# Performance work log

Hardware: AMD Instinct MI355X
Metric: run time of the kernel (lower is better)

## Reference

```python
import jax, jax.numpy as jnp
import numpy as np

N = 50000
E = 500000
HID = 128
H = 4
D = HID // H
NUM_EDGE_TYPES = 8
EPS_LN = 1e-5


def setup_inputs() -> dict:
    key = jax.random.key(0)
    ks = jax.random.split(key, 16)
    s = 1.0 / np.sqrt(HID)
    return {
        "node_embeddings": jax.random.normal(ks[0], (N, HID), jnp.float32),
        "edge_index": jax.random.randint(ks[1], (2, E), 0, N, jnp.int32),
        "edge_type": jax.random.randint(ks[2], (E,), 0, NUM_EDGE_TYPES, jnp.int32),
        "task_embedding": jax.random.normal(ks[3], (HID,), jnp.float32),
        "W_src": jax.random.normal(ks[4], (HID, HID), jnp.float32) * s,
        "b_src": jnp.zeros((HID,), jnp.float32),
        "W_dst": jax.random.normal(ks[5], (HID, HID), jnp.float32) * s,
        "b_dst": jnp.zeros((HID,), jnp.float32),
        "edge_emb": jax.random.normal(ks[6], (NUM_EDGE_TYPES, HID), jnp.float32),
        "att": jax.random.normal(ks[7], (H, D), jnp.float32) * s,
        "W_out": jax.random.normal(ks[8], (HID, HID), jnp.float32) * s,
        "b_out": jnp.zeros((HID,), jnp.float32),
        "norm_w": jnp.ones((HID,), jnp.float32),
        "norm_b": jnp.zeros((HID,), jnp.float32),
        "W_film": jax.random.normal(ks[9], (HID, 2 * HID), jnp.float32) * s,
        "b_film": jnp.zeros((2 * HID,), jnp.float32),
    }


def reference(node_embeddings, edge_index, edge_type, task_embedding,
              W_src, b_src, W_dst, b_dst, edge_emb, att,
              W_out, b_out, norm_w, norm_b, W_film, b_film):
    num_nodes = node_embeddings.shape[0]
    src, dst = edge_index[0], edge_index[1]

    # Node projections -> [N, H, D]
    x_src = (node_embeddings @ W_src + b_src).reshape(num_nodes, H, D)
    x_dst = (node_embeddings @ W_dst + b_dst).reshape(num_nodes, H, D)
    e = edge_emb[edge_type].reshape(-1, H, D)  # [E, H, D]

    # GATv2 attention logits per edge per head
    combined = jax.nn.leaky_relu(x_src[src] + x_dst[dst] + e, negative_slope=0.2)
    logits = jnp.einsum('ehd,hd->eh', combined, att)  # [E, H]

    # Scatter-softmax over destination nodes
    mx = jax.ops.segment_max(logits, dst, num_segments=num_nodes)  # [N, H]
    mx = jnp.where(jnp.isinf(mx), jnp.zeros_like(mx), mx)
    ex = jnp.exp(logits - mx[dst])
    sums = jax.ops.segment_sum(ex, dst, num_segments=num_nodes)  # [N, H]
    attn = ex / jnp.maximum(sums[dst], 1e-12)  # [E, H]

    # Weighted message aggregation
    msg = x_src[src] * attn[..., None]  # [E, H, D]
    agg = jax.ops.segment_sum(msg, dst, num_segments=num_nodes)  # [N, H, D]
    agg = agg.reshape(num_nodes, HID) @ W_out + b_out

    # Task FiLM modulation
    film = task_embedding @ W_film + b_film  # [2*HID]
    gamma, beta = film[:HID], film[HID:]
    agg = agg * (1.0 + 0.5 * jnp.tanh(gamma))[None, :] + beta[None, :]

    # Residual + LayerNorm
    y = node_embeddings + agg
    mu = jnp.mean(y, axis=-1, keepdims=True)
    var = jnp.mean((y - mu) ** 2, axis=-1, keepdims=True)
    return (y - mu) / jnp.sqrt(var + EPS_LN) * norm_w + norm_b
```

## Files before the change

### kernel.cpp

```cpp
#include <hip/hip_runtime.h>
#include <hip/hip_bf16.h>

#define N_NODES 50000
#define E_EDGES 500000
#define HID 128
#define NHEAD 4
#define HDIM 32
#define SCAN_BLOCKS ((N_NODES + 255) / 256)

typedef __attribute__((ext_vector_type(8))) short bf16x8;
typedef __attribute__((ext_vector_type(8))) unsigned short u16x8;
typedef __attribute__((ext_vector_type(4))) float f32x4;

static __device__ __forceinline__ float b2f(unsigned short u) {
    return __uint_as_float((unsigned int)u << 16);
}
static __device__ __forceinline__ unsigned short f2b(float f) {
    unsigned int u = __float_as_uint(f);
    u += 0x7FFFu + ((u >> 16) & 1u);
    return (unsigned short)(u >> 16);
}

__global__ __launch_bounds__(256) void film_kernel(
    const float* __restrict__ task, const float* __restrict__ Wf,
    const float* __restrict__ bf, float* __restrict__ film)
{
    __shared__ float tsk[HID];
    const int t = threadIdx.x;
    if (t < HID) tsk[t] = task[t];
    __syncthreads();
    float acc = bf[t];
    #pragma unroll 8
    for (int k = 0; k < HID; ++k)
        acc = fmaf(tsk[k], Wf[k * 256 + t], acc);
    if (t < HID) film[t] = 1.f + 0.5f * tanhf(acc);
    else         film[t] = acc;
}

__global__ __launch_bounds__(256) void prep_weights(
    const float* __restrict__ Ws, const float* __restrict__ Wd,
    unsigned short* __restrict__ B1)
{
    const int id = blockIdx.x * 256 + threadIdx.x;
    const int n = id >> 7;
    const int k = id & 127;
    const float v = (n < HID) ? Ws[(size_t)k * HID + n]
                              : Wd[(size_t)k * HID + (n - HID)];
    size_t byte = ((size_t)n * HID + k) * 2;
    byte ^= (size_t)((n & 7) << 4);
    *(unsigned short*)((char*)B1 + byte) = f2b(v);
}

__global__ __launch_bounds__(256) void gemm_mfma(
    const float* __restrict__ A, const unsigned short* __restrict__ B1,
    const float* __restrict__ bs, const float* __restrict__ bd,
    unsigned short* __restrict__ xs, unsigned short* __restrict__ xd)
{
    __shared__ unsigned short a_lds[64 * HID];
    __shared__ unsigned short b_lds[256 * HID];
    const int t  = threadIdx.x;
    const int nb = blockIdx.x * 64;

    #pragma unroll
    for (int i = 0; i < 8; ++i) {
        const int f   = t + 256 * i;
        const int row = f >> 5;
        const int k4  = f & 31;
        const int node = nb + row;
        float4 v;
        if (node < N_NODES) v = *(const float4*)(A + (size_t)node * HID + k4 * 4);
        else { v.x = v.y = v.z = v.w = 0.f; }
        ushort4 h;
        h.x = f2b(v.x); h.y = f2b(v.y); h.z = f2b(v.z); h.w = f2b(v.w);
        int byte = row * 256 + k4 * 8;
        byte ^= (row & 7) << 4;
        *(ushort4*)((char*)a_lds + byte) = h;
    }
    #pragma unroll
    for (int i = 0; i < 16; ++i) {
        const int off = (t + 256 * i) * 8;
        const u16x8 v = *(const u16x8*)(B1 + off);
        *(u16x8*)(b_lds + off) = v;
    }
    __syncthreads();

    const int w   = t >> 6;
    const int l   = t & 63;
    const int l15 = l & 15;
    const int kg  = l >> 4;

    f32x4 acc[4][4];
    #pragma unroll
    for (int mf = 0; mf < 4; ++mf)
        #pragma unroll
        for (int nf = 0; nf < 4; ++nf) acc[mf][nf] = (f32x4){0.f, 0.f, 0.f, 0.f};

    #pragma unroll
    for (int ks = 0; ks < 4; ++ks) {
        bf16x8 af[4], bfg[4];
        #pragma unroll
        for (int mf = 0; mf < 4; ++mf) {
            const int r = mf * 16 + l15;
            int byte = r * 256 + ks * 64 + kg * 16;
            byte ^= (r & 7) << 4;
            af[mf] = *(const bf16x8*)((const char*)a_lds + byte);
        }
        #pragma unroll
        for (int nf = 0; nf < 4; ++nf) {
            const int rb = w * 64 + nf * 16 + l15;
            int byte = rb * 256 + ks * 64 + kg * 16;
            byte ^= (rb & 7) << 4;
            bfg[nf] = *(const bf16x8*)((const char*)b_lds + byte);
        }
        #pragma unroll
        for (int mf = 0; mf < 4; ++mf)
            #pragma unroll
            for (int nf = 0; nf < 4; ++nf)
                acc[mf][nf] = __builtin_amdgcn_mfma_f32_16x16x32_bf16(
                    af[mf], bfg[nf], acc[mf][nf], 0, 0, 0);
    }

    float bias[4];
    #pragma unroll
    for (int nf = 0; nf < 4; ++nf) {
        const int col = w * 64 + nf * 16 + l15;
        bias[nf] = (col < HID) ? bs[col] : bd[col - HID];
    }

    __syncthreads();
    unsigned short* c_lds = b_lds;

    #pragma unroll
    for (int mf = 0; mf < 4; ++mf)
        #pragma unroll
        for (int nf = 0; nf < 4; ++nf) {
            const int col = w * 64 + nf * 16 + l15;
            #pragma unroll
            for (int j = 0; j < 4; ++j) {
                const int row = mf * 16 + kg * 4 + j;
                c_lds[row * 264 + col] = f2b(acc[mf][nf][j] + bias[nf]);
            }
        }
    __syncthreads();

    #pragma unroll
    for (int p = 0; p < 8; ++p) {
        const int row   = p * 8 + (t >> 5);
        const int chunk = t & 31;
        const int node  = nb + row;
        if (node < N_NODES) {
            const u16x8 v = *(const u16x8*)(c_lds + row * 264 + chunk * 8);
            if (chunk < 16)
                *(u16x8*)(xs + (size_t)node * HID + chunk * 8) = v;
            else
                *(u16x8*)(xd + (size_t)node * HID + (chunk - 16) * 8) = v;
        }
    }
}

__global__ __launch_bounds__(256) void hist_kernel(
    const int* __restrict__ ei, int* __restrict__ deg)
{
    const int e = blockIdx.x * 256 + threadIdx.x;
    if (e < E_EDGES) atomicAdd(&deg[ei[E_EDGES + e]], 1);
}

__global__ __launch_bounds__(256) void reduce_blocks(
    const int* __restrict__ deg, int* __restrict__ blocksum)
{
    __shared__ int ws_[4];
    const int t = threadIdx.x;
    const int i = blockIdx.x * 256 + t;
    int v = (i < N_NODES) ? deg[i] : 0;
    #pragma unroll
    for (int off = 32; off; off >>= 1) v += __shfl_down(v, off);
    if ((t & 63) == 0) ws_[t >> 6] = v;
    __syncthreads();
    if (t == 0) blocksum[blockIdx.x] = ws_[0] + ws_[1] + ws_[2] + ws_[3];
}

__global__ __launch_bounds__(256) void scan_blocksums(
    const int* __restrict__ blocksum, int* __restrict__ blockoff,
    int* __restrict__ rowptr)
{
    __shared__ int wtot[4];
    const int t    = threadIdx.x;
    const int lane = t & 63;
    const int w    = t >> 6;
    int v = (t < SCAN_BLOCKS) ? blocksum[t] : 0;
    const int own = v;
    #pragma unroll
    for (int off = 1; off < 64; off <<= 1) {
        const int u = __shfl_up(v, off);
        if (lane >= off) v += u;
    }
    if (lane == 63) wtot[w] = v;
    __syncthreads();
    int woff = 0;
    #pragma unroll
    for (int k = 0; k < 4; ++k) if (k < w) woff += wtot[k];
    if (t < SCAN_BLOCKS) blockoff[t] = woff + v - own;
    if (t == 0) rowptr[N_NODES] = E_EDGES;
}

__global__ __launch_bounds__(256) void scan_within(
    const int* __restrict__ deg, const int* __restrict__ blockoff,
    int* __restrict__ rowptr, int* __restrict__ cursor)
{
    __shared__ int wtot[4];
    const int t    = threadIdx.x;
    const int lane = t & 63;
    const int w    = t >> 6;
    const int i    = blockIdx.x * 256 + t;
    int v = (i < N_NODES) ? deg[i] : 0;
    const int own = v;
    #pragma unroll
    for (int off = 1; off < 64; off <<= 1) {
        const int u = __shfl_up(v, off);
        if (lane >= off) v += u;
    }
    if (lane == 63) wtot[w] = v;
    __syncthreads();
    int woff = blockoff[blockIdx.x];
    #pragma unroll
    for (int k = 0; k < 4; ++k) if (k < w) woff += wtot[k];
    if (i < N_NODES) {
        const int ex = woff + v - own;
        rowptr[i] = ex;
        cursor[i] = ex;
    }
}

__global__ __launch_bounds__(256) void scatter_kernel(
    const int* __restrict__ ei, const int* __restrict__ et,
    int* __restrict__ cursor, int* __restrict__ pack)
{
    const int e = blockIdx.x * 256 + threadIdx.x;
    if (e < E_EDGES) {
        const int d = ei[E_EDGES + e];
        const int pos = atomicAdd(&cursor[d], 1);
        pack[pos] = ei[e] | (et[e] << 16);
    }
}

__global__ __launch_bounds__(256) void gather_agg(
    const int* __restrict__ rowptr, const int* __restrict__ pack,
    const unsigned short* __restrict__ xsrc,
    const unsigned short* __restrict__ xdst,
    const float* __restrict__ eemb, const float* __restrict__ att,
    float* __restrict__ agg)
{
    const int lane = threadIdx.x & 31;
    const int grp  = threadIdx.x >> 5;
    const int node = blockIdx.x * 8 + grp;
    if (node >= N_NODES) return;

    const float4 av = *(const float4*)(att + lane * 4);
    const ushort4 xdu = *(const ushort4*)(xdst + (size_t)node * HID + lane * 4);
    const float xdx = b2f(xdu.x), xdy = b2f(xdu.y),
                xdz = b2f(xdu.z), xdw = b2f(xdu.w);

    float a0 = 0.f, a1 = 0.f, a2 = 0.f, a3 = 0.f, sum = 0.f;
    const int b = rowptr[node];
    const int e = rowptr[node + 1];

    int i = b;
    for (; i + 1 < e; i += 2) {
        const int pk0 = pack[i];
        const int pk1 = pack[i + 1];
        const int s0 = pk0 & 0xFFFF, ty0 = pk0 >> 16;
        const int s1 = pk1 & 0xFFFF, ty1 = pk1 >> 16;
        const ushort4 u0 = *(const ushort4*)(xsrc + (size_t)s0 * HID + lane * 4);
        const float4  ev0 = *(const float4*)(eemb + (size_t)ty0 * HID + lane * 4);
        const ushort4 u1 = *(const ushort4*)(xsrc + (size_t)s1 * HID + lane * 4);
        const float4  ev1 = *(const float4*)(eemb + (size_t)ty1 * HID + lane * 4);
        const float x0x = b2f(u0.x), x0y = b2f(u0.y), x0z = b2f(u0.z), x0w = b2f(u0.w);
        const float x1x = b2f(u1.x), x1y = b2f(u1.y), x1z = b2f(u1.z), x1w = b2f(u1.w);
        float c, p0 = 0.f, p1 = 0.f;
        c = x0x + xdx + ev0.x; c = (c > 0.f) ? c : 0.2f * c; p0 = fmaf(c, av.x, p0);
        c = x0y + xdy + ev0.y; c = (c > 0.f) ? c : 0.2f * c; p0 = fmaf(c, av.y, p0);
        c = x0z + xdz + ev0.z; c = (c > 0.f) ? c : 0.2f * c; p0 = fmaf(c, av.z, p0);
        c = x0w + xdw + ev0.w; c = (c > 0.f) ? c : 0.2f * c; p0 = fmaf(c, av.w, p0);
        c = x1x + xdx + ev1.x; c = (c > 0.f) ? c : 0.2f * c; p1 = fmaf(c, av.x, p1);
        c = x1y + xdy + ev1.y; c = (c > 0.f) ? c : 0.2f * c; p1 = fmaf(c, av.y, p1);
        c = x1z + xdz + ev1.z; c = (c > 0.f) ? c : 0.2f * c; p1 = fmaf(c, av.z, p1);
        c = x1w + xdw + ev1.w; c = (c > 0.f) ? c : 0.2f * c; p1 = fmaf(c, av.w, p1);
        p0 += __shfl_xor(p0, 1); p1 += __shfl_xor(p1, 1);
        p0 += __shfl_xor(p0, 2); p1 += __shfl_xor(p1, 2);
        p0 += __shfl_xor(p0, 4); p1 += __shfl_xor(p1, 4);
        const float ex0 = expf(p0);
        const float ex1 = expf(p1);
        a0 = fmaf(ex0, x0x, a0); a1 = fmaf(ex0, x0y, a1);
        a2 = fmaf(ex0, x0z, a2); a3 = fmaf(ex0, x0w, a3);
        a0 = fmaf(ex1, x1x, a0); a1 = fmaf(ex1, x1y, a1);
        a2 = fmaf(ex1, x1z, a2); a3 = fmaf(ex1, x1w, a3);
        sum += ex0 + ex1;
    }
    if (i < e) {
        const int pk0 = pack[i];
        const int s0 = pk0 & 0xFFFF, ty0 = pk0 >> 16;
        const ushort4 u0 = *(const ushort4*)(xsrc + (size_t)s0 * HID + lane * 4);
        const float4  ev0 = *(const float4*)(eemb + (size_t)ty0 * HID + lane * 4);
        const float x0x = b2f(u0.x), x0y = b2f(u0.y), x0z = b2f(u0.z), x0w = b2f(u0.w);
        float c, p0 = 0.f;
        c = x0x + xdx + ev0.x; c = (c > 0.f) ? c : 0.2f * c; p0 = fmaf(c, av.x, p0);
        c = x0y + xdy + ev0.y; c = (c > 0.f) ? c : 0.2f * c; p0 = fmaf(c, av.y, p0);
        c = x0z + xdz + ev0.z; c = (c > 0.f) ? c : 0.2f * c; p0 = fmaf(c, av.z, p0);
        c = x0w + xdw + ev0.w; c = (c > 0.f) ? c : 0.2f * c; p0 = fmaf(c, av.w, p0);
        p0 += __shfl_xor(p0, 1);
        p0 += __shfl_xor(p0, 2);
        p0 += __shfl_xor(p0, 4);
        const float ex0 = expf(p0);
        a0 = fmaf(ex0, x0x, a0); a1 = fmaf(ex0, x0y, a1);
        a2 = fmaf(ex0, x0z, a2); a3 = fmaf(ex0, x0w, a3);
        sum += ex0;
    }

    const float inv = 1.f / fmaxf(sum, 1e-12f);
    float4 o;
    o.x = a0 * inv; o.y = a1 * inv; o.z = a2 * inv; o.w = a3 * inv;
    *(float4*)(agg + (size_t)node * HID + lane * 4) = o;
}

__global__ __launch_bounds__(256) void finalize(
    const float* __restrict__ agg,
    const float* __restrict__ A,   const float* __restrict__ Wo,
    const float* __restrict__ bo,  const float* __restrict__ film,
    const float* __restrict__ nw_, const float* __restrict__ nb_,
    float* __restrict__ out)
{
    __shared__ float a_tile[64][HID];
    const int t  = threadIdx.x;
    const int nb = blockIdx.x * 64;

    #pragma unroll
    for (int i = 0; i < 8; ++i) {
        int f  = t + 256 * i;
        int m  = f >> 5;
        int k4 = f & 31;
        int node = nb + m;
        float4 v;
        if (node < N_NODES) v = *(const float4*)(agg + (size_t)node * HID + k4 * 4);
        else { v.x = v.y = v.z = v.w = 0.f; }
        *(float4*)&a_tile[m][k4 * 4] = v;
    }
    __syncthreads();

    const int cg = t & 31;
    const int rg = t >> 5;
    const int cc = cg * 4;
    const int m0 = rg * 8;

    float acc[8][4];
    #pragma unroll
    for (int m = 0; m < 8; ++m)
        #pragma unroll
        for (int j = 0; j < 4; ++j) acc[m][j] = 0.f;

    for (int kc = 0; kc < 32; ++kc) {
        const int k0 = kc * 4;
        const float4 w0 = *(const float4*)(Wo + (size_t)(k0 + 0) * HID + cc);
        const float4 w1 = *(const float4*)(Wo + (size_t)(k0 + 1) * HID + cc);
        const float4 w2 = *(const float4*)(Wo + (size_t)(k0 + 2) * HID + cc);
        const float4 w3 = *(const float4*)(Wo + (size_t)(k0 + 3) * HID + cc);
        #pragma unroll
        for (int m = 0; m < 8; ++m) {
            const float4 av = *(const float4*)&a_tile[m0 + m][k0];
            acc[m][0] = fmaf(av.x, w0.x, acc[m][0]);
            acc[m][1] = fmaf(av.x, w0.y, acc[m][1]);
            acc[m][2] = fmaf(av.x, w0.z, acc[m][2]);
            acc[m][3] = fmaf(av.x, w0.w, acc[m][3]);
            acc[m][0] = fmaf(av.y, w1.x, acc[m][0]);
            acc[m][1] = fmaf(av.y, w1.y, acc[m][1]);
            acc[m][2] = fmaf(av.y, w1.z, acc[m][2]);
            acc[m][3] = fmaf(av.y, w1.w, acc[m][3]);
            acc[m][0] = fmaf(av.z, w2.x, acc[m][0]);
            acc[m][1] = fmaf(av.z, w2.y, acc[m][1]);
            acc[m][2] = fmaf(av.z, w2.z, acc[m][2]);
            acc[m][3] = fmaf(av.z, w2.w, acc[m][3]);
            acc[m][0] = fmaf(av.w, w3.x, acc[m][0]);
            acc[m][1] = fmaf(av.w, w3.y, acc[m][1]);
            acc[m][2] = fmaf(av.w, w3.z, acc[m][2]);
            acc[m][3] = fmaf(av.w, w3.w, acc[m][3]);
        }
    }

    const float4 bv  = *(const float4*)(bo   + cc);
    const float4 gfv = *(const float4*)(film + cc);
    const float4 btv = *(const float4*)(film + HID + cc);
    const float4 nwv = *(const float4*)(nw_  + cc);
    const float4 nbv = *(const float4*)(nb_  + cc);

    #pragma unroll
    for (int m = 0; m < 8; ++m) {
        const int node = nb + m0 + m;
        float4 y;
        float4 r;
        if (node < N_NODES) r = *(const float4*)(A + (size_t)node * HID + cc);
        else { r.x = r.y = r.z = r.w = 0.f; }
        y.x = fmaf(acc[m][0] + bv.x, gfv.x, btv.x) + r.x;
        y.y = fmaf(acc[m][1] + bv.y, gfv.y, btv.y) + r.y;
        y.z = fmaf(acc[m][2] + bv.z, gfv.z, btv.z) + r.z;
        y.w = fmaf(acc[m][3] + bv.w, gfv.w, btv.w) + r.w;

        float s1 = y.x + y.y + y.z + y.w;
        float s2 = y.x * y.x + y.y * y.y + y.z * y.z + y.w * y.w;
        #pragma unroll
        for (int off = 1; off < 32; off <<= 1) {
            s1 += __shfl_xor(s1, off);
            s2 += __shfl_xor(s2, off);
        }
        const float mu   = s1 * (1.f / 128.f);
        const float var  = s2 * (1.f / 128.f) - mu * mu;
        const float rsig = rsqrtf(var + 1e-5f);
        if (node < N_NODES) {
            float4 o;
            o.x = (y.x - mu) * rsig * nwv.x + nbv.x;
            o.y = (y.y - mu) * rsig * nwv.y + nbv.y;
            o.z = (y.z - mu) * rsig * nwv.z + nbv.z;
            o.w = (y.w - mu) * rsig * nwv.w + nbv.w;
            *(float4*)(out + (size_t)node * HID + cc) = o;
        }
    }
}

extern "C" void kernel_launch(void* const* d_in, const int* in_sizes, int n_in,
                              void* d_out, int out_size, void* d_ws, size_t ws_size,
                              hipStream_t stream)
{
    const float* node_emb = (const float*)d_in[0];
    const int*   edge_idx = (const int*)  d_in[1];
    const int*   edge_ty  = (const int*)  d_in[2];
    const float* task     = (const float*)d_in[3];
    const float* W_src    = (const float*)d_in[4];
    const float* b_src    = (const float*)d_in[5];
    const float* W_dst    = (const float*)d_in[6];
    const float* b_dst    = (const float*)d_in[7];
    const float* edge_emb = (const float*)d_in[8];
    const float* att      = (const float*)d_in[9];
    const float* W_out    = (const float*)d_in[10];
    const float* b_out    = (const float*)d_in[11];
    const float* norm_w   = (const float*)d_in[12];
    const float* norm_b   = (const float*)d_in[13];
    const float* W_film   = (const float*)d_in[14];
    const float* b_film   = (const float*)d_in[15];
    float* out = (float*)d_out;

    char* ws = (char*)d_ws;
    float* agg      = (float*)ws;                            ws += (size_t)N_NODES * HID * 4;
    float* film     = (float*)ws;                            ws += 256 * 4;
    int*   deg      = (int*)ws;                              ws += (size_t)N_NODES * 4;
    int*   rowptr   = (int*)ws;                              ws += (size_t)(N_NODES + 4) * 4;
    int*   cursor   = (int*)ws;                              ws += (size_t)N_NODES * 4;
    int*   blocksum = (int*)ws;                              ws += 256 * 4;
    int*   blockoff = (int*)ws;                              ws += 256 * 4;
    int*   pack     = (int*)ws;                              ws += (size_t)E_EDGES * 4;
    unsigned short* x_src = (unsigned short*)ws;             ws += (size_t)N_NODES * HID * 2;
    unsigned short* x_dst = (unsigned short*)ws;             ws += (size_t)N_NODES * HID * 2;
    unsigned short* wb1   = (unsigned short*)ws;             ws += (size_t)256 * HID * 2;

    hipMemsetAsync(deg, 0, (size_t)N_NODES * sizeof(int), stream);

    film_kernel<<<1, 256, 0, stream>>>(task, W_film, b_film, film);
    hist_kernel<<<(E_EDGES + 255) / 256, 256, 0, stream>>>(edge_idx, deg);
    prep_weights<<<(256 * HID) / 256, 256, 0, stream>>>(W_src, W_dst, wb1);
    gemm_mfma<<<(N_NODES + 63) / 64, 256, 0, stream>>>(
        node_emb, wb1, b_src, b_dst, x_src, x_dst);
    reduce_blocks<<<SCAN_BLOCKS, 256, 0, stream>>>(deg, blocksum);
    scan_blocksums<<<1, 256, 0, stream>>>(blocksum, blockoff, rowptr);
    scan_within<<<SCAN_BLOCKS, 256, 0, stream>>>(deg, blockoff, rowptr, cursor);
    scatter_kernel<<<(E_EDGES + 255) / 256, 256, 0, stream>>>(
        edge_idx, edge_ty, cursor, pack);
    gather_agg<<<(N_NODES + 7) / 8, 256, 0, stream>>>(
        rowptr, pack, x_src, x_dst, edge_emb, att, agg);
    finalize<<<(N_NODES + 63) / 64, 256, 0, stream>>>(
        agg, node_emb, W_out, b_out, film, norm_w, norm_b, out);
}
```

Before: 255.8 us.

## Use split-bf16 MFMA for output projection and merge prep kernels

Moves the finalize kernel's fp32 scalar GEMM onto MFMA using a hi/lo bf16 split (three MFMAs per tile) with pre-transposed, swizzled W_out halves prepared once. Merges the film and weight-prep kernels into a single launch, and makes the histogram and scatter kernels process two edges per thread with int2 loads. Also replaces the leaky-relu select with fmaxf. The split-bf16 product drops the lo*lo term, so results differ slightly from fp32, and finalize now uses more LDS.

```diff
diff --git a/kernel.cpp b/kernel.cpp
--- a/kernel.cpp
+++ b/kernel.cpp
@@ -5,7 +5,6 @@
 #define E_EDGES 500000
 #define HID 128
 #define NHEAD 4
-#define HDIM 32
 #define SCAN_BLOCKS ((N_NODES + 255) / 256)
 
 typedef __attribute__((ext_vector_type(8))) short bf16x8;
@@ -21,34 +20,57 @@
     return (unsigned short)(u >> 16);
 }
 
-__global__ __launch_bounds__(256) void film_kernel(
+__global__ __launch_bounds__(256) void prep_kernel(
+    const float* __restrict__ Ws, const float* __restrict__ Wd,
+    const float* __restrict__ Wo,
     const float* __restrict__ task, const float* __restrict__ Wf,
-    const float* __restrict__ bf, float* __restrict__ film)
-{
-    __shared__ float tsk[HID];
+    const float* __restrict__ bfi,
+    unsigned short* __restrict__ B1,
+    unsigned short* __restrict__ B2h, unsigned short* __restrict__ B2l,
+    float* __restrict__ film)
+{
+    const int blk = blockIdx.x;
     const int t = threadIdx.x;
-    if (t < HID) tsk[t] = task[t];
-    __syncthreads();
-    float acc = bf[t];
-    #pragma unroll 8
-    for (int k = 0; k < HID; ++k)
-        acc = fmaf(tsk[k], Wf[k * 256 + t], acc);
-    if (t < HID) film[t] = 1.f + 0.5f * tanhf(acc);
-    else         film[t] = acc;
-}
-
-__global__ __launch_bounds__(256) void prep_weights(
-    const float* __restrict__ Ws, const float* __restrict__ Wd,
-    unsigned short* __restrict__ B1)
-{
-    const int id = blockIdx.x * 256 + threadIdx.x;
-    const int n = id >> 7;
-    const int k = id & 127;
-    const float v = (n < HID) ? Ws[(size_t)k * HID + n]
-                              : Wd[(size_t)k * HID + (n - HID)];
-    size_t byte = ((size_t)n * HID + k) * 2;
-    byte ^= (size_t)((n & 7) << 4);
-    *(unsigned short*)((char*)B1 + byte) = f2b(v);
+    if (blk < 256) {
+        const int id = blk * 256 + t;
+        if (id < 256 * HID) {
+            const int n = id >> 7;
+            const int k = id & 127;
+            const float v = (n < HID) ? Ws[(size_t)k * HID + n]
+                                      : Wd[(size_t)k * HID + (n - HID)];
+            size_t byte = ((size_t)n * HID + k) * 2;
+            byte ^= (size_t)((n & 7) << 4);
+            *(unsigned short*)((char*)B1 + byte) = f2b(v);
+        } else if (id < 256 * HID + HID * HID) {
+            const int id2 = id - 256 * HID;
+            const int n = id2 >> 7;
+            const int k = id2 & 127;
+            const float v = Wo[(size_t)k * HID + n];
+            size_t byte = ((size_t)n * HID + k) * 2;
+            byte ^= (size_t)((n & 7) << 4);
+            *(unsigned short*)((char*)B2h + byte) = f2b(v);
+        } else {
+            const int id3 = id - 256 * HID - HID * HID;
+            const int n = id3 >> 7;
+            const int k = id3 & 127;
+            const float v = Wo[(size_t)k * HID + n];
+            const unsigned short hi = f2b(v);
+            const unsigned short lo = f2b(v - b2f(hi));
+            size_t byte = ((size_t)n * HID + k) * 2;
+            byte ^= (size_t)((n & 7) << 4);
+            *(unsigned short*)((char*)B2l + byte) = lo;
+        }
+    } else {
+        __shared__ float tsk[HID];
+        if (t < HID) tsk[t] = task[t];
+        __syncthreads();
+        float acc = bfi[t];
+        #pragma unroll 8
+        for (int k = 0; k < HID; ++k)
+            acc = fmaf(tsk[k], Wf[k * 256 + t], acc);
+        if (t < HID) film[t] = 1.f + 0.5f * tanhf(acc);
+        else         film[t] = acc;
+    }
 }
 
 __global__ __launch_bounds__(256) void gemm_mfma(
@@ -161,8 +183,13 @@
 __global__ __launch_bounds__(256) void hist_kernel(
     const int* __restrict__ ei, int* __restrict__ deg)
 {
-    const int e = blockIdx.x * 256 + threadIdx.x;
-    if (e < E_EDGES) atomicAdd(&deg[ei[E_EDGES + e]], 1);
+    const int e2 = blockIdx.x * 256 + threadIdx.x;
+    const int e = e2 * 2;
+    if (e < E_EDGES) {
+        const int2 d = *(const int2*)(ei + E_EDGES + e);
+        atomicAdd(&deg[d.x], 1);
+        if (e + 1 < E_EDGES) atomicAdd(&deg[d.y], 1);
+    }
 }
 
 __global__ __launch_bounds__(256) void reduce_blocks(
@@ -235,11 +262,18 @@
     const int* __restrict__ ei, const int* __restrict__ et,
     int* __restrict__ cursor, int* __restrict__ pack)
 {
-    const int e = blockIdx.x * 256 + threadIdx.x;
+    const int e2 = blockIdx.x * 256 + threadIdx.x;
+    const int e = e2 * 2;
     if (e < E_EDGES) {
-        const int d = ei[E_EDGES + e];
-        const int pos = atomicAdd(&cursor[d], 1);
-        pack[pos] = ei[e] | (et[e] << 16);
+        const int2 s  = *(const int2*)(ei + e);
+        const int2 d  = *(const int2*)(ei + E_EDGES + e);
+        const int2 ty = *(const int2*)(et + e);
+        const int p0 = atomicAdd(&cursor[d.x], 1);
+        pack[p0] = s.x | (ty.x << 16);
+        if (e + 1 < E_EDGES) {
+            const int p1 = atomicAdd(&cursor[d.y], 1);
+            pack[p1] = s.y | (ty.y << 16);
+        }
     }
 }
 
@@ -277,14 +311,14 @@
         const float x0x = b2f(u0.x), x0y = b2f(u0.y), x0z = b2f(u0.z), x0w = b2f(u0.w);
         const float x1x = b2f(u1.x), x1y = b2f(u1.y), x1z = b2f(u1.z), x1w = b2f(u1.w);
         float c, p0 = 0.f, p1 = 0.f;
-        c = x0x + xdx + ev0.x; c = (c > 0.f) ? c : 0.2f * c; p0 = fmaf(c, av.x, p0);
-        c = x0y + xdy + ev0.y; c = (c > 0.f) ? c : 0.2f * c; p0 = fmaf(c, av.y, p0);
-        c = x0z + xdz + ev0.z; c = (c > 0.f) ? c : 0.2f * c; p0 = fmaf(c, av.z, p0);
-        c = x0w + xdw + ev0.w; c = (c > 0.f) ? c : 0.2f * c; p0 = fmaf(c, av.w, p0);
-        c = x1x + xdx + ev1.x; c = (c > 0.f) ? c : 0.2f * c; p1 = fmaf(c, av.x, p1);
-        c = x1y + xdy + ev1.y; c = (c > 0.f) ? c : 0.2f * c; p1 = fmaf(c, av.y, p1);
-        c = x1z + xdz + ev1.z; c = (c > 0.f) ? c : 0.2f * c; p1 = fmaf(c, av.z, p1);
-        c = x1w + xdw + ev1.w; c = (c > 0.f) ? c : 0.2f * c; p1 = fmaf(c, av.w, p1);
+        c = x0x + xdx + ev0.x; c = fmaxf(c, 0.2f * c); p0 = fmaf(c, av.x, p0);
+        c = x0y + xdy + ev0.y; c = fmaxf(c, 0.2f * c); p0 = fmaf(c, av.y, p0);
+        c = x0z + xdz + ev0.z; c = fmaxf(c, 0.2f * c); p0 = fmaf(c, av.z, p0);
+        c = x0w + xdw + ev0.w; c = fmaxf(c, 0.2f * c); p0 = fmaf(c, av.w, p0);
+        c = x1x + xdx + ev1.x; c = fmaxf(c, 0.2f * c); p1 = fmaf(c, av.x, p1);
+        c = x1y + xdy + ev1.y; c = fmaxf(c, 0.2f * c); p1 = fmaf(c, av.y, p1);
+        c = x1z + xdz + ev1.z; c = fmaxf(c, 0.2f * c); p1 = fmaf(c, av.z, p1);
+        c = x1w + xdw + ev1.w; c = fmaxf(c, 0.2f * c); p1 = fmaf(c, av.w, p1);
         p0 += __shfl_xor(p0, 1); p1 += __shfl_xor(p1, 1);
         p0 += __shfl_xor(p0, 2); p1 += __shfl_xor(p1, 2);
         p0 += __shfl_xor(p0, 4); p1 += __shfl_xor(p1, 4);
@@ -303,10 +337,10 @@
         const float4  ev0 = *(const float4*)(eemb + (size_t)ty0 * HID + lane * 4);
         const float x0x = b2f(u0.x), x0y = b2f(u0.y), x0z = b2f(u0.z), x0w = b2f(u0.w);
         float c, p0 = 0.f;
-        c = x0x + xdx + ev0.x; c = (c > 0.f) ? c : 0.2f * c; p0 = fmaf(c, av.x, p0);
-        c = x0y + xdy + ev0.y; c = (c > 0.f) ? c : 0.2f * c; p0 = fmaf(c, av.y, p0);
-        c = x0z + xdz + ev0.z; c = (c > 0.f) ? c : 0.2f * c; p0 = fmaf(c, av.z, p0);
-        c = x0w + xdw + ev0.w; c = (c > 0.f) ? c : 0.2f * c; p0 = fmaf(c, av.w, p0);
+        c = x0x + xdx + ev0.x; c = fmaxf(c, 0.2f * c); p0 = fmaf(c, av.x, p0);
+        c = x0y + xdy + ev0.y; c = fmaxf(c, 0.2f * c); p0 = fmaf(c, av.y, p0);
+        c = x0z + xdz + ev0.z; c = fmaxf(c, 0.2f * c); p0 = fmaf(c, av.z, p0);
+        c = x0w + xdw + ev0.w; c = fmaxf(c, 0.2f * c); p0 = fmaf(c, av.w, p0);
         p0 += __shfl_xor(p0, 1);
         p0 += __shfl_xor(p0, 2);
         p0 += __shfl_xor(p0, 4);
@@ -324,66 +358,112 @@
 
 __global__ __launch_bounds__(256) void finalize(
     const float* __restrict__ agg,
-    const float* __restrict__ A,   const float* __restrict__ Wo,
-    const float* __restrict__ bo,  const float* __restrict__ film,
+    const unsigned short* __restrict__ B2h,
+    const unsigned short* __restrict__ B2l,
+    const float* __restrict__ A,   const float* __restrict__ bo,
+    const float* __restrict__ film,
     const float* __restrict__ nw_, const float* __restrict__ nb_,
     float* __restrict__ out)
 {
-    __shared__ float a_tile[64][HID];
+    __shared__ unsigned short a_hi[64 * HID];
+    __shared__ unsigned short a_lo[64 * HID];
+    __shared__ __align__(16) unsigned short b_pair[2 * HID * HID];
+    float* c_lds = (float*)b_pair;
+    unsigned short* b_hi = b_pair;
+    unsigned short* b_lo = b_pair + HID * HID;
+
     const int t  = threadIdx.x;
     const int nb = blockIdx.x * 64;
 
     #pragma unroll
     for (int i = 0; i < 8; ++i) {
-        int f  = t + 256 * i;
-        int m  = f >> 5;
-        int k4 = f & 31;
-        int node = nb + m;
+        const int f   = t + 256 * i;
+        const int row = f >> 5;
+        const int k4  = f & 31;
+        const int node = nb + row;
         float4 v;
         if (node < N_NODES) v = *(const float4*)(agg + (size_t)node * HID + k4 * 4);
         else { v.x = v.y = v.z = v.w = 0.f; }
-        *(float4*)&a_tile[m][k4 * 4] = v;
-    }
+        ushort4 h, lo;
+        h.x = f2b(v.x); lo.x = f2b(v.x - b2f(h.x));
+        h.y = f2b(v.y); lo.y = f2b(v.y - b2f(h.y));
+        h.z = f2b(v.z); lo.z = f2b(v.z - b2f(h.z));
+        h.w = f2b(v.w); lo.w = f2b(v.w - b2f(h.w));
+        int byte = row * 256 + k4 * 8;
+        byte ^= (row & 7) << 4;
+        *(ushort4*)((char*)a_hi + byte) = h;
+        *(ushort4*)((char*)a_lo + byte) = lo;
+    }
+    #pragma unroll
+    for (int i = 0; i < 8; ++i) {
+        const int off = (t + 256 * i) * 8;
+        *(u16x8*)(b_hi + off) = *(const u16x8*)(B2h + off);
+        *(u16x8*)(b_lo + off) = *(const u16x8*)(B2l + off);
+    }
+    __syncthreads();
+
+    const int w   = t >> 6;
+    const int l   = t & 63;
+    const int l15 = l & 15;
+    const int kg  = l >> 4;
+
+    f32x4 acc[4][2];
+    #pragma unroll
+    for (int mf = 0; mf < 4; ++mf)
+        #pragma unroll
+        for (int nf = 0; nf < 2; ++nf) acc[mf][nf] = (f32x4){0.f, 0.f, 0.f, 0.f};
+
+    #pragma unroll
+    for (int ks = 0; ks < 4; ++ks) {
+        bf16x8 afh[4], afl[4], bfh[2], bfl[2];
+        #pragma unroll
+        for (int mf = 0; mf < 4; ++mf) {
+            const int r = mf * 16 + l15;
+            int byte = r * 256 + ks * 64 + kg * 16;
+            byte ^= (r & 7) << 4;
+            afh[mf] = *(const bf16x8*)((const char*)a_hi + byte);
+            afl[mf] = *(const bf16x8*)((const char*)a_lo + byte);
+        }
+        #pragma unroll
+        for (int nf = 0; nf < 2; ++nf) {
+            const int rb = w * 32 + nf * 16 + l15;
+            int byte = rb * 256 + ks * 64 + kg * 16;
+            byte ^= (rb & 7) << 4;
+            bfh[nf] = *(const bf16x8*)((const char*)b_hi + byte);
+            bfl[nf] = *(const bf16x8*)((const char*)b_lo + byte);
+        }
+        #pragma unroll
+        for (int mf = 0; mf < 4; ++mf)
+            #pragma unroll
+            for (int nf = 0; nf < 2; ++nf) {
+                acc[mf][nf] = __builtin_amdgcn_mfma_f32_16x16x32_bf16(
+                    afh[mf], bfh[nf], acc[mf][nf], 0, 0, 0);
+                acc[mf][nf] = __builtin_amdgcn_mfma_f32_16x16x32_bf16(
+                    afh[mf], bfl[nf], acc[mf][nf], 0, 0, 0);
+                acc[mf][nf] = __builtin_amdgcn_mfma_f32_16x16x32_bf16(
+                    afl[mf], bfh[nf], acc[mf][nf], 0, 0, 0);
+            }
+    }
+
+    __syncthreads();
+
+    #pragma unroll
+    for (int mf = 0; mf < 4; ++mf)
+        #pragma unroll
+        for (int nf = 0; nf < 2; ++nf) {
+            const int col = w * 32 + nf * 16 + l15;
+            #pragma unroll
+            for (int j = 0; j < 4; ++j) {
+                const int row = mf * 16 + kg * 4 + j;
+                c_lds[row * 132 + col] = acc[mf][nf][j];
+            }
+        }
     __syncthreads();
 
     const int cg = t & 31;
     const int rg = t >> 5;
     const int cc = cg * 4;
     const int m0 = rg * 8;
-
-    float acc[8][4];
-    #pragma unroll
-    for (int m = 0; m < 8; ++m)
-        #pragma unroll
-        for (int j = 0; j < 4; ++j) acc[m][j] = 0.f;
-
-    for (int kc = 0; kc < 32; ++kc) {
-        const int k0 = kc * 4;
-        const float4 w0 = *(const float4*)(Wo + (size_t)(k0 + 0) * HID + cc);
-        const float4 w1 = *(const float4*)(Wo + (size_t)(k0 + 1) * HID + cc);
-        const float4 w2 = *(const float4*)(Wo + (size_t)(k0 + 2) * HID + cc);
-        const float4 w3 = *(const float4*)(Wo + (size_t)(k0 + 3) * HID + cc);
-        #pragma unroll
-        for (int m = 0; m < 8; ++m) {
-            const float4 av = *(const float4*)&a_tile[m0 + m][k0];
-            acc[m][0] = fmaf(av.x, w0.x, acc[m][0]);
-            acc[m][1] = fmaf(av.x, w0.y, acc[m][1]);
-            acc[m][2] = fmaf(av.x, w0.z, acc[m][2]);
-            acc[m][3] = fmaf(av.x, w0.w, acc[m][3]);
-            acc[m][0] = fmaf(av.y, w1.x, acc[m][0]);
-            acc[m][1] = fmaf(av.y, w1.y, acc[m][1]);
-            acc[m][2] = fmaf(av.y, w1.z, acc[m][2]);
-            acc[m][3] = fmaf(av.y, w1.w, acc[m][3]);
-            acc[m][0] = fmaf(av.z, w2.x, acc[m][0]);
-            acc[m][1] = fmaf(av.z, w2.y, acc[m][1]);
-            acc[m][2] = fmaf(av.z, w2.z, acc[m][2]);
-            acc[m][3] = fmaf(av.z, w2.w, acc[m][3]);
-            acc[m][0] = fmaf(av.w, w3.x, acc[m][0]);
-            acc[m][1] = fmaf(av.w, w3.y, acc[m][1]);
-            acc[m][2] = fmaf(av.w, w3.z, acc[m][2]);
-            acc[m][3] = fmaf(av.w, w3.w, acc[m][3]);
-        }
-    }
 
     const float4 bv  = *(const float4*)(bo   + cc);
     const float4 gfv = *(const float4*)(film + cc);
@@ -393,15 +473,17 @@
 
     #pragma unroll
     for (int m = 0; m < 8; ++m) {
-        const int node = nb + m0 + m;
-        float4 y;
+        const int row  = m0 + m;
+        const int node = nb + row;
+        const float4 cv = *(const float4*)&c_lds[row * 132 + cc];
         float4 r;
         if (node < N_NODES) r = *(const float4*)(A + (size_t)node * HID + cc);
         else { r.x = r.y = r.z = r.w = 0.f; }
-        y.x = fmaf(acc[m][0] + bv.x, gfv.x, btv.x) + r.x;
-        y.y = fmaf(acc[m][1] + bv.y, gfv.y, btv.y) + r.y;
-        y.z = fmaf(acc[m][2] + bv.z, gfv.z, btv.z) + r.z;
-        y.w = fmaf(acc[m][3] + bv.w, gfv.w, btv.w) + r.w;
+        float4 y;
+        y.x = fmaf(cv.x + bv.x, gfv.x, btv.x) + r.x;
+        y.y = fmaf(cv.y + bv.y, gfv.y, btv.y) + r.y;
+        y.z = fmaf(cv.z + bv.z, gfv.z, btv.z) + r.z;
+        y.w = fmaf(cv.w + bv.w, gfv.w, btv.w) + r.w;
 
         float s1 = y.x + y.y + y.z + y.w;
         float s2 = y.x * y.x + y.y * y.y + y.z * y.z + y.w * y.w;
@@ -458,21 +540,23 @@
     unsigned short* x_src = (unsigned short*)ws;             ws += (size_t)N_NODES * HID * 2;
     unsigned short* x_dst = (unsigned short*)ws;             ws += (size_t)N_NODES * HID * 2;
     unsigned short* wb1   = (unsigned short*)ws;             ws += (size_t)256 * HID * 2;
+    unsigned short* wb2h  = (unsigned short*)ws;             ws += (size_t)HID * HID * 2;
+    unsigned short* wb2l  = (unsigned short*)ws;             ws += (size_t)HID * HID * 2;
 
     hipMemsetAsync(deg, 0, (size_t)N_NODES * sizeof(int), stream);
 
-    film_kernel<<<1, 256, 0, stream>>>(task, W_film, b_film, film);
-    hist_kernel<<<(E_EDGES + 255) / 256, 256, 0, stream>>>(edge_idx, deg);
-    prep_weights<<<(256 * HID) / 256, 256, 0, stream>>>(W_src, W_dst, wb1);
+    prep_kernel<<<257, 256, 0, stream>>>(
+        W_src, W_dst, W_out, task, W_film, b_film, wb1, wb2h, wb2l, film);
+    hist_kernel<<<(E_EDGES / 2 + 255) / 256, 256, 0, stream>>>(edge_idx, deg);
     gemm_mfma<<<(N_NODES + 63) / 64, 256, 0, stream>>>(
         node_emb, wb1, b_src, b_dst, x_src, x_dst);
     reduce_blocks<<<SCAN_BLOCKS, 256, 0, stream>>>(deg, blocksum);
     scan_blocksums<<<1, 256, 0, stream>>>(blocksum, blockoff, rowptr);
     scan_within<<<SCAN_BLOCKS, 256, 0, stream>>>(deg, blockoff, rowptr, cursor);
-    scatter_kernel<<<(E_EDGES + 255) / 256, 256, 0, stream>>>(
+    scatter_kernel<<<(E_EDGES / 2 + 255) / 256, 256, 0, stream>>>(
         edge_idx, edge_ty, cursor, pack);
     gather_agg<<<(N_NODES + 7) / 8, 256, 0, stream>>>(
         rowptr, pack, x_src, x_dst, edge_emb, att, agg);
     finalize<<<(N_NODES + 63) / 64, 256, 0, stream>>>(
-        agg, node_emb, W_out, b_out, film, norm_w, norm_b, out);
-}
+        agg, wb2h, wb2l, node_emb, b_out, film, norm_w, norm_b, out);
+}
```

After: 257.7 us. Within noise of the previous version (+0.7%).
